# Kernel tuning notes

Hardware: AMD Instinct MI355X
Metric: run time of the kernel (lower is better)

## Reference

```python
import jax, jax.numpy as jnp
import numpy as np

B = 32          # batch_size
M = 1024        # mesh_num (nodes per sub-graph)
D_IN = 128      # sub_node_feature_input_dim
D_OUT = 128     # sub_node_feature_output_dim
E_DIM = 64      # embedding dim per node


def setup_inputs() -> dict:
    key = jax.random.key(0)
    k1, k2, k3, k4 = jax.random.split(key, 4)
    return {
        "node_feature_group": jax.random.normal(k1, (B * M, D_IN), dtype=jnp.float32),
        "embedding_group": jax.random.normal(k2, (B * M, E_DIM), dtype=jnp.float32),
        "W1": jax.random.normal(k3, (D_OUT, D_IN), dtype=jnp.float32) * (1.0 / np.sqrt(D_IN)),
        "W2": jax.random.normal(k4, (D_OUT, D_OUT), dtype=jnp.float32) * (1.0 / np.sqrt(D_OUT)),
    }


def reference(node_feature_group, embedding_group, W1, W2):
    # The torch module builds a (B*M)x(B*M) block-diagonal adjacency via
    # torch.block_diag; off-block entries are exactly zero, and row sums /
    # D^-1/2 A D^-1/2 normalization act per block, so we compute per-graph.
    E = embedding_group.reshape(B, M, E_DIM)
    adj = jnp.maximum(jnp.einsum('bme,bne->bmn', E, E), 0.0)  # clamp(E E^T, 0)
    adj = adj + jnp.eye(M, dtype=adj.dtype)                   # A = adj + I
    d = adj.sum(-1)                                           # [B, M]
    dinv = d ** -0.5                                          # symmetric=True
    dad = dinv[:, :, None] * adj * dinv[:, None, :]           # D^-1/2 A D^-1/2

    X = node_feature_group.reshape(B, M, D_IN)
    y = jax.nn.relu(jnp.einsum('bmn,bnd->bmd', dad, X) @ W1.T)   # gcn1
    y = jax.nn.relu(jnp.einsum('bmn,bnd->bmd', dad, y) @ W2.T)   # gcn2
    # Dropout is identity in eval mode.
    return y.reshape(B * M, D_OUT)
```

## Files before the change

### kernel.cpp

```cpp
#include <hip/hip_runtime.h>
#include <stdint.h>

#define B_  32
#define M_  1024
#define DF  128
#define ED  64

typedef __attribute__((ext_vector_type(8))) short short8;
typedef __attribute__((ext_vector_type(4))) short short4v;
typedef __attribute__((ext_vector_type(4))) float floatx4;

__device__ inline unsigned short f2bf(float f) {
    union { float f; unsigned u; } v; v.f = f;
    unsigned r = v.u + 0x7fffu + ((v.u >> 16) & 1u);
    return (unsigned short)(r >> 16);
}

__device__ inline short8 cvt8(float4 a, float4 b) {
    short8 s;
    s[0] = (short)f2bf(a.x); s[1] = (short)f2bf(a.y);
    s[2] = (short)f2bf(a.z); s[3] = (short)f2bf(a.w);
    s[4] = (short)f2bf(b.x); s[5] = (short)f2bf(b.y);
    s[6] = (short)f2bf(b.z); s[7] = (short)f2bf(b.w);
    return s;
}

__device__ inline void load_lds16(const void* g, void* l) {
    __builtin_amdgcn_global_load_lds(
        (const __attribute__((address_space(1))) unsigned int*)g,
        (__attribute__((address_space(3))) unsigned int*)l, 16, 0, 0);
}

__global__ __launch_bounds__(256) void build_fused_kernel(
    const float* __restrict__ E, const float* __restrict__ X,
    unsigned short* __restrict__ S, float* __restrict__ dinv,
    unsigned short* __restrict__ Xt) {
    int mt2 = blockIdx.x, b = blockIdx.y;
    int t = threadIdx.x;
    int w = t >> 6, lane = t & 63, quad = lane >> 4, lc = lane & 15;
    int m0 = mt2 * 64;

    __shared__ unsigned short sEn[128 * 72];
    __shared__ unsigned short sOt[128 * 72];
    __shared__ float sDinv[64];

    const float* Eb = E + (size_t)b * M_ * ED;
    unsigned short* Sg = S + ((size_t)b << 20);
    int base_m = m0 + w * 16;

    short8 afr[2];
    for (int ks = 0; ks < 2; ++ks) {
        const float* p = Eb + (size_t)(base_m + lc) * ED + ks * 32 + quad * 8;
        afr[ks] = cvt8(*(const float4*)p, *(const float4*)(p + 4));
    }
    floatx4 rsum = (floatx4){0.f, 0.f, 0.f, 0.f};

    for (int nc = 0; nc < 8; ++nc) {
        __syncthreads();
        for (int it = 0; it < 4; ++it) {
            int c = t + 256 * it;
            int row = c >> 3, off = (c & 7) * 8;
            const float* p = Eb + (size_t)(nc * 128 + row) * ED + off;
            *(short8*)(&sEn[row * 72 + off]) = cvt8(*(const float4*)p, *(const float4*)(p + 4));
        }
        __syncthreads();
        for (int nt = 0; nt < 8; ++nt) {
            short8 b0 = *(const short8*)(&sEn[(nt * 16 + lc) * 72 + quad * 8]);
            short8 b1 = *(const short8*)(&sEn[(nt * 16 + lc) * 72 + 32 + quad * 8]);
            floatx4 s = (floatx4){0.f, 0.f, 0.f, 0.f};
            s = __builtin_amdgcn_mfma_f32_16x16x32_bf16(afr[0], b0, s, 0, 0, 0);
            s = __builtin_amdgcn_mfma_f32_16x16x32_bf16(afr[1], b1, s, 0, 0, 0);
            int nloc = nt * 16 + lc;
            int n = nc * 128 + nloc;
            short4v pk;
            for (int r = 0; r < 4; ++r) {
                int m = base_m + quad * 4 + r;
                float v = fmaxf(s[r], 0.f);
                if (m == n) v += 1.0f;
                rsum[r] += v;
                pk[r] = (short)f2bf(v);
            }
            *(short4v*)(&sOt[nloc * 72 + w * 16 + quad * 4]) = pk;
        }
        __syncthreads();
        for (int it = 0; it < 4; ++it) {
            int c = t + 256 * it;
            int row = c >> 3, off = (c & 7) * 8;
            *(short8*)(Sg + (size_t)(nc * 128 + row) * M_ + m0 + off) =
                *(const short8*)(&sOt[row * 72 + off]);
        }
    }
    for (int r = 0; r < 4; ++r) {
        float v = rsum[r];
        v += __shfl_xor(v, 1, 16);
        v += __shfl_xor(v, 2, 16);
        v += __shfl_xor(v, 4, 16);
        v += __shfl_xor(v, 8, 16);
        if (lc == 0) {
            float dvv = rsqrtf(v);
            int mloc = w * 16 + quad * 4 + r;
            sDinv[mloc] = dvv;
            dinv[b * M_ + m0 + mloc] = dvv;
        }
    }
    __syncthreads();
    {
        int nloc = t >> 5;
        int d4 = (t & 31) * 4;
        for (int pass = 0; pass < 8; ++pass) {
            int n = pass * 8 + nloc;
            float sc = sDinv[n];
            float4 v = *(const float4*)(X + (size_t)(b * M_ + m0 + n) * DF + d4);
            sOt[(d4 + 0) * 72 + n] = f2bf(v.x * sc);
            sOt[(d4 + 1) * 72 + n] = f2bf(v.y * sc);
            sOt[(d4 + 2) * 72 + n] = f2bf(v.z * sc);
            sOt[(d4 + 3) * 72 + n] = f2bf(v.w * sc);
        }
    }
    __syncthreads();
    for (int it = 0; it < 4; ++it) {
        int c = t + 256 * it;
        int d = c >> 3, off = (c & 7) * 8;
        *(short8*)(Xt + (size_t)(b * DF + d) * M_ + m0 + off) =
            *(const short8*)(&sOt[d * 72 + off]);
    }
}

template <int MODE>
__global__ __launch_bounds__(256) void gemm_kernel(
    const unsigned short* __restrict__ S,
    const unsigned short* __restrict__ Pt,
    const float* __restrict__ Wf,
    const float* __restrict__ dinv,
    unsigned short* __restrict__ OutT,
    float* __restrict__ OutF) {
    int bx = blockIdx.x, b = blockIdx.y;
    int m0 = bx * 64;
    int t = threadIdx.x;
    int w = t >> 6, lane = t & 63, quad = lane >> 4, lc = lane & 15;
    int wr = w & 1, wc = w >> 1;

    __shared__ unsigned short lds[26112];
    unsigned short* sA = lds;
    unsigned short* sB = lds + 4096;
    unsigned short* sY = lds;
    unsigned short* sW = lds + 8704;

    const unsigned short* Sg = S + ((size_t)b << 20);
    const unsigned short* Pb = Pt + (size_t)b * DF * M_;

    floatx4 acc[2][4];
    for (int i = 0; i < 2; ++i)
        for (int j = 0; j < 4; ++j) acc[i][j] = (floatx4){0.f, 0.f, 0.f, 0.f};

    for (int nc = 0; nc < 16; ++nc) {
        __syncthreads();
        for (int r = 0; r < 2; ++r) {
            int te = r * 256 + w * 64 + lane;
            const void* gp = Sg + (size_t)(m0 + (te >> 3)) * M_ + nc * 64 + (te & 7) * 8;
            load_lds16(gp, (char*)sA + (r * 256 + w * 64) * 16);
        }
        for (int r = 0; r < 4; ++r) {
            int te = r * 256 + w * 64 + lane;
            const void* gp = Pb + (size_t)(te >> 3) * M_ + nc * 64 + (te & 7) * 8;
            load_lds16(gp, (char*)sB + (r * 256 + w * 64) * 16);
        }
        __syncthreads();
        for (int ks = 0; ks < 2; ++ks) {
            short8 afr[2], bfr[4];
            for (int i = 0; i < 2; ++i)
                afr[i] = *(const short8*)(&sA[(wr * 32 + i * 16 + lc) * 64 + ks * 32 + quad * 8]);
            for (int j = 0; j < 4; ++j)
                bfr[j] = *(const short8*)(&sB[(wc * 64 + j * 16 + lc) * 64 + ks * 32 + quad * 8]);
            for (int i = 0; i < 2; ++i)
                for (int j = 0; j < 4; ++j)
                    acc[i][j] = __builtin_amdgcn_mfma_f32_16x16x32_bf16(afr[i], bfr[j], acc[i][j], 0, 0, 0);
        }
    }

    float dv[2][4];
    for (int i = 0; i < 2; ++i)
        for (int r = 0; r < 4; ++r)
            dv[i][r] = dinv[b * M_ + m0 + wr * 32 + i * 16 + quad * 4 + r];
    __syncthreads();
    for (int i = 0; i < 2; ++i)
        for (int j = 0; j < 4; ++j) {
            int mrow = wr * 32 + i * 16 + quad * 4;
            int col = wc * 64 + j * 16 + lc;
            for (int r = 0; r < 4; ++r)
                sY[(mrow + r) * 136 + col] = f2bf(acc[i][j][r] * dv[i][r]);
        }
    for (int it = 0; it < 8; ++it) {
        int c = t + 256 * it;
        int row = c >> 4, off = (c & 15) * 8;
        const float* p = Wf + row * DF + off;
        *(short8*)(&sW[row * 136 + off]) = cvt8(*(const float4*)p, *(const float4*)(p + 4));
    }
    __syncthreads();
    floatx4 accH[2][4];
    for (int i = 0; i < 2; ++i)
        for (int j = 0; j < 4; ++j) accH[i][j] = (floatx4){0.f, 0.f, 0.f, 0.f};
    for (int ks = 0; ks < 4; ++ks) {
        short8 afr[2], bfr[4];
        for (int i = 0; i < 2; ++i)
            afr[i] = *(const short8*)(&sY[(wr * 32 + i * 16 + lc) * 136 + ks * 32 + quad * 8]);
        for (int j = 0; j < 4; ++j)
            bfr[j] = *(const short8*)(&sW[(wc * 64 + j * 16 + lc) * 136 + ks * 32 + quad * 8]);
        for (int i = 0; i < 2; ++i)
            for (int j = 0; j < 4; ++j)
                accH[i][j] = __builtin_amdgcn_mfma_f32_16x16x32_bf16(afr[i], bfr[j], accH[i][j], 0, 0, 0);
    }
    if (MODE == 2) {
        __syncthreads();
        float* sF = (float*)lds;
        for (int i = 0; i < 2; ++i)
            for (int j = 0; j < 4; ++j) {
                int mrow = wr * 32 + i * 16 + quad * 4;
                int col = wc * 64 + j * 16 + lc;
                for (int r = 0; r < 4; ++r)
                    sF[(mrow + r) * 132 + col] = fmaxf(accH[i][j][r], 0.f);
            }
        __syncthreads();
        float* Ob = OutF + ((size_t)b * M_ + m0) * DF;
        for (int it = 0; it < 8; ++it) {
            int c = t + 256 * it;
            int row = c >> 5, off = (c & 31) * 4;
            *(float4*)(Ob + (size_t)row * DF + off) = *(const float4*)(&sF[row * 132 + off]);
        }
    } else {
        __syncthreads();
        unsigned short* sT = sW;
        for (int i = 0; i < 2; ++i)
            for (int j = 0; j < 4; ++j) {
                int mrow = wr * 32 + i * 16 + quad * 4;
                int col = wc * 64 + j * 16 + lc;
                short4v pk;
                for (int r = 0; r < 4; ++r)
                    pk[r] = (short)f2bf(fmaxf(accH[i][j][r], 0.f) * dv[i][r]);
                *(short4v*)(&sT[col * 72 + mrow]) = pk;
            }
        __syncthreads();
        for (int it = 0; it < 4; ++it) {
            int c = t + 256 * it;
            int o = c >> 3, off = (c & 7) * 8;
            *(short8*)(OutT + (size_t)(b * DF + o) * M_ + m0 + off) =
                *(const short8*)(&sT[o * 72 + off]);
        }
    }
}

__global__ __launch_bounds__(256) void cast_kernel(
    const float* __restrict__ E, const float* __restrict__ W1,
    const float* __restrict__ W2, unsigned short* __restrict__ Ebf,
    unsigned short* __restrict__ W1bf, unsigned short* __restrict__ W2bf) {
    const int NE = B_ * M_ * ED;
    const int NW = DF * DF;
    int idx = (blockIdx.x * 256 + threadIdx.x) * 4;
    const float* src; unsigned short* dst; int off;
    if (idx < NE)            { src = E;  dst = Ebf;  off = idx; }
    else if (idx < NE + NW)  { src = W1; dst = W1bf; off = idx - NE; }
    else                     { src = W2; dst = W2bf; off = idx - NE - NW; }
    float4 v = *(const float4*)(src + off);
    ushort4 o;
    o.x = f2bf(v.x); o.y = f2bf(v.y); o.z = f2bf(v.z); o.w = f2bf(v.w);
    *(ushort4*)(dst + off) = o;
}

__global__ __launch_bounds__(256) void degree_kernel(
    const unsigned short* __restrict__ Ebf, float* __restrict__ dinv) {
    int mt = blockIdx.x, b = blockIdx.y;
    int t = threadIdx.x;
    int w = t >> 6, lane = t & 63, quad = lane >> 4, lc = lane & 15;
    __shared__ unsigned short sEn[128][72];
    const unsigned short* Eb = Ebf + (size_t)b * M_ * ED;
    short8 afr[2][2];
    for (int i = 0; i < 2; ++i) {
        int row = mt * 128 + w * 32 + i * 16 + lc;
        for (int ks = 0; ks < 2; ++ks)
            afr[i][ks] = *(const short8*)(Eb + (size_t)row * ED + ks * 32 + quad * 8);
    }
    floatx4 rsum[2];
    rsum[0] = (floatx4){0.f,0.f,0.f,0.f};
    rsum[1] = (floatx4){0.f,0.f,0.f,0.f};
    for (int nc = 0; nc < 8; ++nc) {
        __syncthreads();
        for (int it = 0; it < 4; ++it) {
            int c = t + 256 * it;
            int row = c >> 3, off = (c & 7) * 8;
            *(short8*)(&sEn[row][off]) =
                *(const short8*)(Eb + (size_t)(nc * 128 + row) * ED + off);
        }
        __syncthreads();
        for (int nt = 0; nt < 8; ++nt) {
            short8 b0 = *(const short8*)(&sEn[nt * 16 + lc][quad * 8]);
            short8 b1 = *(const short8*)(&sEn[nt * 16 + lc][32 + quad * 8]);
            for (int i = 0; i < 2; ++i) {
                floatx4 s = (floatx4){0.f,0.f,0.f,0.f};
                s = __builtin_amdgcn_mfma_f32_16x16x32_bf16(afr[i][0], b0, s, 0, 0, 0);
                s = __builtin_amdgcn_mfma_f32_16x16x32_bf16(afr[i][1], b1, s, 0, 0, 0);
                for (int r = 0; r < 4; ++r) rsum[i][r] += fmaxf(s[r], 0.f);
            }
        }
    }
    for (int i = 0; i < 2; ++i)
        for (int r = 0; r < 4; ++r) {
            float v = rsum[i][r];
            v += __shfl_xor(v, 1, 16);
            v += __shfl_xor(v, 2, 16);
            v += __shfl_xor(v, 4, 16);
            v += __shfl_xor(v, 8, 16);
            if (lc == 0) {
                int row = mt * 128 + w * 32 + i * 16 + quad * 4 + r;
                dinv[b * M_ + row] = rsqrtf(1.0f + v);
            }
        }
}

__global__ __launch_bounds__(256) void tscale128_kernel(
    const float* __restrict__ X, const float* __restrict__ dinv,
    unsigned short* __restrict__ Xt) {
    int mt = blockIdx.x, b = blockIdx.y;
    int t = threadIdx.x;
    __shared__ unsigned short sT[128][136];
    int nloc = t >> 5;
    int d4 = (t & 31) * 4;
    for (int pass = 0; pass < 16; ++pass) {
        int n = pass * 8 + nloc;
        int grow = b * M_ + mt * 128 + n;
        float sc = dinv[grow];
        float4 v = *(const float4*)(X + (size_t)grow * DF + d4);
        sT[d4 + 0][n] = f2bf(v.x * sc);
        sT[d4 + 1][n] = f2bf(v.y * sc);
        sT[d4 + 2][n] = f2bf(v.z * sc);
        sT[d4 + 3][n] = f2bf(v.w * sc);
    }
    __syncthreads();
    for (int it = 0; it < 8; ++it) {
        int c = t + 256 * it;
        int d = c >> 4, off = (c & 15) * 8;
        *(short8*)(Xt + (size_t)(b * DF + d) * M_ + mt * 128 + off) =
            *(const short8*)(&sT[d][off]);
    }
}

template <int MODE>
__global__ __launch_bounds__(256) void gcn_kernel(
    const unsigned short* __restrict__ Ebf,
    const unsigned short* __restrict__ Pt,
    const unsigned short* __restrict__ Wbf,
    const float* __restrict__ dinv,
    unsigned short* __restrict__ OutT,
    float* __restrict__ OutF) {
    int mt = blockIdx.x, b = blockIdx.y;
    int t = threadIdx.x;
    int w = t >> 6, lane = t & 63, quad = lane >> 4, lc = lane & 15;
    int wr = w & 1, wc = w >> 1;
    __shared__ unsigned short sEn[128][72];
    __shared__ unsigned short sS[128][136];
    __shared__ unsigned short sPW[128][136];
    const unsigned short* Eb = Ebf + (size_t)b * M_ * ED;
    short8 ae[4][2];
    for (int i = 0; i < 4; ++i) {
        int row = mt * 128 + wr * 64 + i * 16 + lc;
        for (int ks = 0; ks < 2; ++ks)
            ae[i][ks] = *(const short8*)(Eb + (size_t)row * ED + ks * 32 + quad * 8);
    }
    floatx4 accZ[4][4];
    for (int i = 0; i < 4; ++i)
        for (int j = 0; j < 4; ++j) accZ[i][j] = (floatx4){0.f,0.f,0.f,0.f};
    for (int nc = 0; nc < 8; ++nc) {
        __syncthreads();
        for (int it = 0; it < 4; ++it) {
            int c = t + 256 * it;
            int row = c >> 3, off = (c & 7) * 8;
            *(short8*)(&sEn[row][off]) =
                *(const short8*)(Eb + (size_t)(nc * 128 + row) * ED + off);
        }
        for (int it = 0; it < 8; ++it) {
            int c = t + 256 * it;
            int drow = c >> 4, off = (c & 15) * 8;
            *(short8*)(&sPW[drow][off]) =
                *(const short8*)(Pt + (size_t)(b * DF + drow) * M_ + nc * 128 + off);
        }
        __syncthreads();
        for (int jt = 0; jt < 4; ++jt) {
            int ncol = wc * 64 + jt * 16;
            short8 b0 = *(const short8*)(&sEn[ncol + lc][quad * 8]);
            short8 b1 = *(const short8*)(&sEn[ncol + lc][32 + quad * 8]);
            for (int i = 0; i < 4; ++i) {
                floatx4 s = (floatx4){0.f,0.f,0.f,0.f};
                s = __builtin_amdgcn_mfma_f32_16x16x32_bf16(ae[i][0], b0, s, 0, 0, 0);
                s = __builtin_amdgcn_mfma_f32_16x16x32_bf16(ae[i][1], b1, s, 0, 0, 0);
                int mrow = wr * 64 + i * 16 + quad * 4;
                for (int r = 0; r < 4; ++r) {
                    float v = fmaxf(s[r], 0.f);
                    if (mt == nc && (mrow + r) == (ncol + lc)) v += 1.0f;
                    sS[mrow + r][ncol + lc] = f2bf(v);
                }
            }
        }
        __syncthreads();
        for (int ks = 0; ks < 4; ++ks) {
            short8 afr[4];
            for (int i = 0; i < 4; ++i)
                afr[i] = *(const short8*)(&sS[wr * 64 + i * 16 + lc][ks * 32 + quad * 8]);
            for (int j = 0; j < 4; ++j) {
                short8 bfr = *(const short8*)(&sPW[wc * 64 + j * 16 + lc][ks * 32 + quad * 8]);
                for (int i = 0; i < 4; ++i)
                    accZ[i][j] = __builtin_amdgcn_mfma_f32_16x16x32_bf16(afr[i], bfr, accZ[i][j], 0, 0, 0);
            }
        }
    }
    float dv[4][4];
    for (int i = 0; i < 4; ++i)
        for (int r = 0; r < 4; ++r)
            dv[i][r] = dinv[b * M_ + mt * 128 + wr * 64 + i * 16 + quad * 4 + r];
    __syncthreads();
    for (int i = 0; i < 4; ++i)
        for (int j = 0; j < 4; ++j) {
            int mrow = wr * 64 + i * 16 + quad * 4;
            int col = wc * 64 + j * 16 + lc;
            for (int r = 0; r < 4; ++r)
                sS[mrow + r][col] = f2bf(accZ[i][j][r] * dv[i][r]);
        }
    for (int it = 0; it < 8; ++it) {
        int c = t + 256 * it;
        int row = c >> 4, off = (c & 15) * 8;
        *(short8*)(&sPW[row][off]) = *(const short8*)(Wbf + row * DF + off);
    }
    __syncthreads();
    floatx4 accH[4][4];
    for (int i = 0; i < 4; ++i)
        for (int j = 0; j < 4; ++j) accH[i][j] = (floatx4){0.f,0.f,0.f,0.f};
    for (int ks = 0; ks < 4; ++ks) {
        short8 afr[4], bfr[4];
        for (int i = 0; i < 4; ++i)
            afr[i] = *(const short8*)(&sS[wr * 64 + i * 16 + lc][ks * 32 + quad * 8]);
        for (int j = 0; j < 4; ++j)
            bfr[j] = *(const short8*)(&sPW[wc * 64 + j * 16 + lc][ks * 32 + quad * 8]);
        for (int i = 0; i < 4; ++i)
            for (int j = 0; j < 4; ++j)
                accH[i][j] = __builtin_amdgcn_mfma_f32_16x16x32_bf16(afr[i], bfr[j], accH[i][j], 0, 0, 0);
    }
    if (MODE == 2) {
        float* Ob = OutF + ((size_t)b * M_ + mt * 128) * DF;
        for (int i = 0; i < 4; ++i)
            for (int j = 0; j < 4; ++j) {
                int mrow = wr * 64 + i * 16 + quad * 4;
                int col = wc * 64 + j * 16 + lc;
                for (int r = 0; r < 4; ++r)
                    Ob[(size_t)(mrow + r) * DF + col] = fmaxf(accH[i][j][r], 0.f);
            }
    } else {
        __syncthreads();
        for (int i = 0; i < 4; ++i)
            for (int j = 0; j < 4; ++j) {
                int mrow = wr * 64 + i * 16 + quad * 4;
                int col = wc * 64 + j * 16 + lc;
                for (int r = 0; r < 4; ++r)
                    sS[col][mrow + r] = f2bf(fmaxf(accH[i][j][r], 0.f) * dv[i][r]);
            }
        __syncthreads();
        unsigned short* Ob = OutT + (size_t)b * DF * M_ + mt * 128;
        for (int it = 0; it < 8; ++it) {
            int c = t + 256 * it;
            int orow = c >> 4, off = (c & 15) * 8;
            *(short8*)(Ob + (size_t)orow * M_ + off) = *(const short8*)(&sS[orow][off]);
        }
    }
}

extern "C" void kernel_launch(void* const* d_in, const int* in_sizes, int n_in,
                              void* d_out, int out_size, void* d_ws, size_t ws_size,
                              hipStream_t stream) {
    (void)in_sizes; (void)n_in; (void)out_size;
    const float* X  = (const float*)d_in[0];
    const float* E  = (const float*)d_in[1];
    const float* W1 = (const float*)d_in[2];
    const float* W2 = (const float*)d_in[3];
    float* out = (float*)d_out;

    char* ws = (char*)d_ws;
    unsigned short* Ebf  = (unsigned short*)(ws);
    unsigned short* W1bf = (unsigned short*)(ws + 4194304);
    unsigned short* W2bf = (unsigned short*)(ws + 4227072);
    float*          dinv = (float*)(ws + 4259840);
    unsigned short* Xt   = (unsigned short*)(ws + 4390912);
    unsigned short* Ht   = (unsigned short*)(ws + 12779520);
    unsigned short* Smat = (unsigned short*)(ws + 21168128);
    const size_t NEED = 21168128ull + 67108864ull;

    if (ws_size >= NEED) {
        build_fused_kernel<<<dim3(16, 32), 256, 0, stream>>>(E, X, Smat, dinv, Xt);
        gemm_kernel<1><<<dim3(16, 32), 256, 0, stream>>>(Smat, Xt, W1, dinv, Ht, nullptr);
        gemm_kernel<2><<<dim3(16, 32), 256, 0, stream>>>(Smat, Ht, W2, dinv, nullptr, out);
    } else {
        cast_kernel<<<2080, 256, 0, stream>>>(E, W1, W2, Ebf, W1bf, W2bf);
        degree_kernel<<<dim3(8, 32), 256, 0, stream>>>(Ebf, dinv);
        tscale128_kernel<<<dim3(8, 32), 256, 0, stream>>>(X, dinv, Xt);
        gcn_kernel<1><<<dim3(8, 32), 256, 0, stream>>>(Ebf, Xt, W1bf, dinv, Ht, nullptr);
        gcn_kernel<2><<<dim3(8, 32), 256, 0, stream>>>(Ebf, Ht, W2bf, dinv, nullptr, out);
    }
}
```

Baseline: 155.5 us.

## Recompute adjacency tiles on the fly instead of materializing the bf16 S matrix

Drops the 64 MB bf16 adjacency matrix the build kernel used to write and each layer kernel read twice. The prep kernel now writes a bf16 copy of E, and each layer kernel rebuilds clamp(E E^T)+I tiles in LDS with MFMA before the aggregation GEMM. Blocks are also remapped so that blocks of the same graph are spread across the grid, likely to improve cache locality or balance. The trade is extra MFMA work (the E E^T recompute in both layers) and higher LDS use per block, which may lower occupancy, in exchange for far less HBM traffic.

```diff
diff --git a/kernel.cpp b/kernel.cpp
--- a/kernel.cpp
+++ b/kernel.cpp
@@ -25,27 +25,27 @@
     return s;
 }
 
-__device__ inline void load_lds16(const void* g, void* l) {
-    __builtin_amdgcn_global_load_lds(
-        (const __attribute__((address_space(1))) unsigned int*)g,
-        (__attribute__((address_space(3))) unsigned int*)l, 16, 0, 0);
-}
-
-__global__ __launch_bounds__(256) void build_fused_kernel(
+__device__ inline void remap_block(int& b, int& mt2) {
+    int lin = blockIdx.y * 16 + blockIdx.x;
+    int g = lin & 7, kk = lin >> 3;
+    b = g * 4 + (kk >> 4);
+    mt2 = kk & 15;
+}
+
+__global__ __launch_bounds__(256) void prep_kernel(
     const float* __restrict__ E, const float* __restrict__ X,
-    unsigned short* __restrict__ S, float* __restrict__ dinv,
+    unsigned short* __restrict__ Ebf, float* __restrict__ dinv,
     unsigned short* __restrict__ Xt) {
-    int mt2 = blockIdx.x, b = blockIdx.y;
+    int b, mt2; remap_block(b, mt2);
+    int m0 = mt2 * 64;
     int t = threadIdx.x;
     int w = t >> 6, lane = t & 63, quad = lane >> 4, lc = lane & 15;
-    int m0 = mt2 * 64;
 
     __shared__ unsigned short sEn[128 * 72];
-    __shared__ unsigned short sOt[128 * 72];
     __shared__ float sDinv[64];
 
     const float* Eb = E + (size_t)b * M_ * ED;
-    unsigned short* Sg = S + ((size_t)b << 20);
+    unsigned short* Ebg = Ebf + (size_t)b * M_ * ED;
     int base_m = m0 + w * 16;
 
     short8 afr[2];
@@ -64,30 +64,28 @@
             *(short8*)(&sEn[row * 72 + off]) = cvt8(*(const float4*)p, *(const float4*)(p + 4));
         }
         __syncthreads();
+        if ((mt2 & 7) == nc) {
+            int half = mt2 >> 3;
+            for (int it = 0; it < 2; ++it) {
+                int c = t + 256 * it;
+                int row = half * 64 + (c >> 3), off = (c & 7) * 8;
+                *(short8*)(Ebg + (size_t)(nc * 128 + row) * ED + off) =
+                    *(const short8*)(&sEn[row * 72 + off]);
+            }
+        }
         for (int nt = 0; nt < 8; ++nt) {
             short8 b0 = *(const short8*)(&sEn[(nt * 16 + lc) * 72 + quad * 8]);
             short8 b1 = *(const short8*)(&sEn[(nt * 16 + lc) * 72 + 32 + quad * 8]);
             floatx4 s = (floatx4){0.f, 0.f, 0.f, 0.f};
             s = __builtin_amdgcn_mfma_f32_16x16x32_bf16(afr[0], b0, s, 0, 0, 0);
             s = __builtin_amdgcn_mfma_f32_16x16x32_bf16(afr[1], b1, s, 0, 0, 0);
-            int nloc = nt * 16 + lc;
-            int n = nc * 128 + nloc;
-            short4v pk;
+            int n = nc * 128 + nt * 16 + lc;
             for (int r = 0; r < 4; ++r) {
                 int m = base_m + quad * 4 + r;
                 float v = fmaxf(s[r], 0.f);
                 if (m == n) v += 1.0f;
                 rsum[r] += v;
-                pk[r] = (short)f2bf(v);
-            }
-            *(short4v*)(&sOt[nloc * 72 + w * 16 + quad * 4]) = pk;
-        }
-        __syncthreads();
-        for (int it = 0; it < 4; ++it) {
-            int c = t + 256 * it;
-            int row = c >> 3, off = (c & 7) * 8;
-            *(short8*)(Sg + (size_t)(nc * 128 + row) * M_ + m0 + off) =
-                *(const short8*)(&sOt[row * 72 + off]);
+            }
         }
     }
     for (int r = 0; r < 4; ++r) {
@@ -111,10 +109,10 @@
             int n = pass * 8 + nloc;
             float sc = sDinv[n];
             float4 v = *(const float4*)(X + (size_t)(b * M_ + m0 + n) * DF + d4);
-            sOt[(d4 + 0) * 72 + n] = f2bf(v.x * sc);
-            sOt[(d4 + 1) * 72 + n] = f2bf(v.y * sc);
-            sOt[(d4 + 2) * 72 + n] = f2bf(v.z * sc);
-            sOt[(d4 + 3) * 72 + n] = f2bf(v.w * sc);
+            sEn[(d4 + 0) * 72 + n] = f2bf(v.x * sc);
+            sEn[(d4 + 1) * 72 + n] = f2bf(v.y * sc);
+            sEn[(d4 + 2) * 72 + n] = f2bf(v.z * sc);
+            sEn[(d4 + 3) * 72 + n] = f2bf(v.w * sc);
         }
     }
     __syncthreads();
@@ -122,56 +120,81 @@
         int c = t + 256 * it;
         int d = c >> 3, off = (c & 7) * 8;
         *(short8*)(Xt + (size_t)(b * DF + d) * M_ + m0 + off) =
-            *(const short8*)(&sOt[d * 72 + off]);
+            *(const short8*)(&sEn[d * 72 + off]);
     }
 }
 
 template <int MODE>
-__global__ __launch_bounds__(256) void gemm_kernel(
-    const unsigned short* __restrict__ S,
+__global__ __launch_bounds__(256) void layer_kernel(
+    const unsigned short* __restrict__ Ebf,
     const unsigned short* __restrict__ Pt,
     const float* __restrict__ Wf,
     const float* __restrict__ dinv,
     unsigned short* __restrict__ OutT,
     float* __restrict__ OutF) {
-    int bx = blockIdx.x, b = blockIdx.y;
-    int m0 = bx * 64;
+    int b, mt2; remap_block(b, mt2);
+    int m0 = mt2 * 64;
     int t = threadIdx.x;
     int w = t >> 6, lane = t & 63, quad = lane >> 4, lc = lane & 15;
     int wr = w & 1, wc = w >> 1;
 
-    __shared__ unsigned short lds[26112];
-    unsigned short* sA = lds;
-    unsigned short* sB = lds + 4096;
-    unsigned short* sY = lds;
-    unsigned short* sW = lds + 8704;
-
-    const unsigned short* Sg = S + ((size_t)b << 20);
+    __shared__ unsigned short lds[35328];
+    unsigned short* sEn = lds;
+    unsigned short* sS  = lds + 9216;
+    unsigned short* sPW = lds + 17920;
+
+    const unsigned short* Eb = Ebf + (size_t)b * M_ * ED;
     const unsigned short* Pb = Pt + (size_t)b * DF * M_;
+
+    short8 ae[2][2];
+    for (int i = 0; i < 2; ++i) {
+        int row = m0 + wr * 32 + i * 16 + lc;
+        for (int ks = 0; ks < 2; ++ks)
+            ae[i][ks] = *(const short8*)(Eb + (size_t)row * ED + ks * 32 + quad * 8);
+    }
 
     floatx4 acc[2][4];
     for (int i = 0; i < 2; ++i)
         for (int j = 0; j < 4; ++j) acc[i][j] = (floatx4){0.f, 0.f, 0.f, 0.f};
 
-    for (int nc = 0; nc < 16; ++nc) {
-        __syncthreads();
-        for (int r = 0; r < 2; ++r) {
-            int te = r * 256 + w * 64 + lane;
-            const void* gp = Sg + (size_t)(m0 + (te >> 3)) * M_ + nc * 64 + (te & 7) * 8;
-            load_lds16(gp, (char*)sA + (r * 256 + w * 64) * 16);
-        }
-        for (int r = 0; r < 4; ++r) {
-            int te = r * 256 + w * 64 + lane;
-            const void* gp = Pb + (size_t)(te >> 3) * M_ + nc * 64 + (te & 7) * 8;
-            load_lds16(gp, (char*)sB + (r * 256 + w * 64) * 16);
-        }
-        __syncthreads();
-        for (int ks = 0; ks < 2; ++ks) {
+    for (int nc = 0; nc < 8; ++nc) {
+        __syncthreads();
+        for (int it = 0; it < 4; ++it) {
+            int c = t + 256 * it;
+            int row = c >> 3, off = (c & 7) * 8;
+            *(short8*)(&sEn[row * 72 + off]) =
+                *(const short8*)(Eb + (size_t)(nc * 128 + row) * ED + off);
+        }
+        for (int it = 0; it < 8; ++it) {
+            int c = t + 256 * it;
+            int drow = c >> 4, off = (c & 15) * 8;
+            *(short8*)(&sPW[drow * 136 + off]) =
+                *(const short8*)(Pb + (size_t)drow * M_ + nc * 128 + off);
+        }
+        __syncthreads();
+        for (int jt = 0; jt < 4; ++jt) {
+            int ncol = wc * 64 + jt * 16;
+            short8 b0 = *(const short8*)(&sEn[(ncol + lc) * 72 + quad * 8]);
+            short8 b1 = *(const short8*)(&sEn[(ncol + lc) * 72 + 32 + quad * 8]);
+            for (int i = 0; i < 2; ++i) {
+                floatx4 s = (floatx4){0.f, 0.f, 0.f, 0.f};
+                s = __builtin_amdgcn_mfma_f32_16x16x32_bf16(ae[i][0], b0, s, 0, 0, 0);
+                s = __builtin_amdgcn_mfma_f32_16x16x32_bf16(ae[i][1], b1, s, 0, 0, 0);
+                int mrow = wr * 32 + i * 16 + quad * 4;
+                for (int r = 0; r < 4; ++r) {
+                    float v = fmaxf(s[r], 0.f);
+                    if (m0 + mrow + r == nc * 128 + ncol + lc) v += 1.0f;
+                    sS[(mrow + r) * 136 + ncol + lc] = f2bf(v);
+                }
+            }
+        }
+        __syncthreads();
+        for (int ks = 0; ks < 4; ++ks) {
             short8 afr[2], bfr[4];
             for (int i = 0; i < 2; ++i)
-                afr[i] = *(const short8*)(&sA[(wr * 32 + i * 16 + lc) * 64 + ks * 32 + quad * 8]);
+                afr[i] = *(const short8*)(&sS[(wr * 32 + i * 16 + lc) * 136 + ks * 32 + quad * 8]);
             for (int j = 0; j < 4; ++j)
-                bfr[j] = *(const short8*)(&sB[(wc * 64 + j * 16 + lc) * 64 + ks * 32 + quad * 8]);
+                bfr[j] = *(const short8*)(&sPW[(wc * 64 + j * 16 + lc) * 136 + ks * 32 + quad * 8]);
             for (int i = 0; i < 2; ++i)
                 for (int j = 0; j < 4; ++j)
                     acc[i][j] = __builtin_amdgcn_mfma_f32_16x16x32_bf16(afr[i], bfr[j], acc[i][j], 0, 0, 0);
@@ -183,6 +206,8 @@
         for (int r = 0; r < 4; ++r)
             dv[i][r] = dinv[b * M_ + m0 + wr * 32 + i * 16 + quad * 4 + r];
     __syncthreads();
+    unsigned short* sY = sS;
+    unsigned short* sW = sPW;
     for (int i = 0; i < 2; ++i)
         for (int j = 0; j < 4; ++j) {
             int mrow = wr * 32 + i * 16 + quad * 4;
@@ -487,13 +512,12 @@
     float*          dinv = (float*)(ws + 4259840);
     unsigned short* Xt   = (unsigned short*)(ws + 4390912);
     unsigned short* Ht   = (unsigned short*)(ws + 12779520);
-    unsigned short* Smat = (unsigned short*)(ws + 21168128);
-    const size_t NEED = 21168128ull + 67108864ull;
+    const size_t NEED = 21168128ull;
 
     if (ws_size >= NEED) {
-        build_fused_kernel<<<dim3(16, 32), 256, 0, stream>>>(E, X, Smat, dinv, Xt);
-        gemm_kernel<1><<<dim3(16, 32), 256, 0, stream>>>(Smat, Xt, W1, dinv, Ht, nullptr);
-        gemm_kernel<2><<<dim3(16, 32), 256, 0, stream>>>(Smat, Ht, W2, dinv, nullptr, out);
+        prep_kernel<<<dim3(16, 32), 256, 0, stream>>>(E, X, Ebf, dinv, Xt);
+        layer_kernel<1><<<dim3(16, 32), 256, 0, stream>>>(Ebf, Xt, W1, dinv, Ht, nullptr);
+        layer_kernel<2><<<dim3(16, 32), 256, 0, stream>>>(Ebf, Ht, W2, dinv, nullptr, out);
     } else {
         cast_kernel<<<2080, 256, 0, stream>>>(E, W1, W2, Ebf, W1bf, W2bf);
         degree_kernel<<<dim3(8, 32), 256, 0, stream>>>(Ebf, dinv);
```

New measurement: 154.1 us. No clear change (-0.9%).
